# Kernel optimization log

Measured on AMD Instinct MI355X. Metric: run time of the kernel, lower is better.

The kernel has to match this reference:

```python
import jax, jax.numpy as jnp
import numpy as np

D_MODEL, D_K, D_V, HEADS = 512, 8, 8, 6
EPS = 1e-5


def setup_inputs() -> dict:
    key = jax.random.key(0)
    ks = jax.random.split(key, 16)
    B, S = 16, 1024
    inp = {
        'q_input': jax.random.normal(ks[0], (B, S, D_MODEL), jnp.float32),
        'k_input': jax.random.normal(ks[1], (B, S, D_MODEL), jnp.float32),
        'v_input': jax.random.normal(ks[2], (B, S, D_MODEL), jnp.float32),
        'mask': jax.random.randint(ks[3], (B, S, S), 0, 2).astype(bool),
        'Wq': jax.random.normal(ks[4], (D_MODEL, D_K * HEADS), jnp.float32) * 0.04,
        'bq': jax.random.normal(ks[5], (D_K * HEADS,), jnp.float32) * 0.02,
        'Wk': jax.random.normal(ks[6], (D_MODEL, D_K * HEADS), jnp.float32) * 0.04,
        'bk': jax.random.normal(ks[7], (D_K * HEADS,), jnp.float32) * 0.02,
        'Wv': jax.random.normal(ks[8], (D_MODEL, D_V * HEADS), jnp.float32) * 0.04,
        'bv': jax.random.normal(ks[9], (D_V * HEADS,), jnp.float32) * 0.02,
        'Wo': jax.random.normal(ks[10], (HEADS * D_K, D_MODEL), jnp.float32) * 0.1,
        'bo': jax.random.normal(ks[11], (D_MODEL,), jnp.float32) * 0.02,
        'ln_w': 1.0 + jax.random.normal(ks[12], (D_MODEL,), jnp.float32) * 0.02,
        'ln_b': jax.random.normal(ks[13], (D_MODEL,), jnp.float32) * 0.02,
    }
    return inp


def reference(q_input, k_input, v_input, mask, Wq, bq, Wk, bk, Wv, bv, Wo, bo, ln_w, ln_b):
    B, S, _ = q_input.shape
    # projections -> [B, H, S, d]
    q_s = (q_input @ Wq + bq).reshape(B, S, HEADS, D_K).transpose(0, 2, 1, 3)
    k_s = (k_input @ Wk + bk).reshape(B, S, HEADS, D_K).transpose(0, 2, 1, 3)
    v_s = (v_input @ Wv + bv).reshape(B, S, HEADS, D_V).transpose(0, 2, 1, 3)
    # scaled dot-product with masked_fill(mask, 1e-9) as in the original (fills VALUE, not -inf)
    scores = jnp.einsum('bhqd,bhkd->bhqk', q_s, k_s) / np.sqrt(D_K).astype(np.float32)
    scores = jnp.where(mask[:, None, :, :], jnp.float32(1e-9), scores)
    attn = jax.nn.softmax(scores, axis=-1)
    out = jnp.einsum('bhqk,bhkd->bhqd', attn, v_s)  # [B,H,S,d_v]
    out = out.transpose(0, 2, 1, 3).reshape(B, S, HEADS * D_K)
    out = out @ Wo + bo
    x = q_input + out  # residual
    mu = jnp.mean(x, axis=-1, keepdims=True)
    var = jnp.var(x, axis=-1, keepdims=True)
    return (x - mu) * jax.lax.rsqrt(var + EPS) * ln_w + ln_b
```

## Files before the change

### kernel.cpp

```cpp
#include <hip/hip_runtime.h>

constexpr int B = 16;
constexpr int S = 1024;
constexpr int DM = 512;
constexpr int H = 6;
constexpr int DK = 8;
constexpr int NJ = H * DK;
constexpr int BS = B * S;
constexpr int WB_ELEMS = 16 * NJ * 32;

typedef __attribute__((ext_vector_type(8))) short bf16x8;
typedef __attribute__((ext_vector_type(8))) _Float16 half8;
typedef __attribute__((ext_vector_type(4))) float floatx4;

#define LOG2E 1.4426950408889634f
#define QSCALE (0.35355339059327373f * LOG2E)

__device__ inline ushort f2bf(float f) {
  unsigned int u = __builtin_bit_cast(unsigned int, f);
  return (ushort)((u + 0x7FFFu + ((u >> 16) & 1u)) >> 16);
}

__global__ __launch_bounds__(256) void maskbits_kernel(
    const int* __restrict__ mask, unsigned long long* __restrict__ bits) {
  int wave = threadIdx.x >> 6, lane = threadIdx.x & 63;
  int row = blockIdx.x * 4 + wave;
  const int* mrow = mask + (size_t)row * S;
  unsigned long long* brow = bits + (size_t)row * 16;
#pragma unroll
  for (int c = 0; c < 16; c++) {
    int v = mrow[c * 64 + lane];
    unsigned long long bal = __ballot(v != 0);
    if (lane == 0) brow[c] = bal;
  }
}

__global__ __launch_bounds__(256) void wprep_kernel(
    const float* __restrict__ Wq, const float* __restrict__ Wk,
    const float* __restrict__ Wv, ushort* __restrict__ Wb) {
  int m = blockIdx.x;
  const float* W = (m == 0) ? Wq : (m == 1) ? Wk : Wv;
  ushort* dst = Wb + (size_t)m * WB_ELEMS;
  for (int e = threadIdx.x; e < WB_ELEMS; e += 256) {
    int kc = e / 1536;
    int rem = e - kc * 1536;
    int n = rem >> 5, kj = rem & 31;
    dst[e] = f2bf(W[(size_t)(kc * 32 + kj) * NJ + n]);
  }
}

__global__ __launch_bounds__(256) void proj_kernel(
    const float* __restrict__ q_in, const float* __restrict__ k_in,
    const float* __restrict__ v_in, const ushort* __restrict__ Wb,
    const float* __restrict__ bq, const float* __restrict__ bk,
    const float* __restrict__ bv,
    ushort* __restrict__ Qo, ushort* __restrict__ Ko, ushort* __restrict__ Vo) {
  int m = blockIdx.y;
  const float* x    = (m == 0) ? q_in : (m == 1) ? k_in : v_in;
  const float* bias = (m == 0) ? bq   : (m == 1) ? bk   : bv;
  ushort* out       = (m == 0) ? Qo   : (m == 1) ? Ko   : Vo;
  float oscale      = (m == 0) ? QSCALE : 1.0f;
  const ushort* Wg  = Wb + (size_t)m * WB_ELEMS;

  __shared__ ushort Wl[WB_ELEMS];

  int t = threadIdx.x;
  {
    const uint4* src = (const uint4*)Wg;
    uint4* dst = (uint4*)Wl;
#pragma unroll
    for (int i = 0; i < 12; i++) dst[t + i * 256] = src[t + i * 256];
  }

  int r0 = blockIdx.x * 64;
  int wave = t >> 6, lane = t & 63;
  int n16 = lane & 15, quad = lane >> 4;
  const float* xrow = x + (size_t)(r0 + wave * 16 + n16) * DM + quad * 8;

  floatx4 acc0 = {0.f, 0.f, 0.f, 0.f};
  floatx4 acc1 = {0.f, 0.f, 0.f, 0.f};
  floatx4 acc2 = {0.f, 0.f, 0.f, 0.f};

  __syncthreads();

#pragma unroll 4
  for (int kc = 0; kc < 16; kc++) {
    float4 xa = *(const float4*)(xrow + kc * 32);
    float4 xb = *(const float4*)(xrow + kc * 32 + 4);
    bf16x8 a;
    a[0] = (short)f2bf(xa.x); a[1] = (short)f2bf(xa.y);
    a[2] = (short)f2bf(xa.z); a[3] = (short)f2bf(xa.w);
    a[4] = (short)f2bf(xb.x); a[5] = (short)f2bf(xb.y);
    a[6] = (short)f2bf(xb.z); a[7] = (short)f2bf(xb.w);
    const ushort* wbase = &Wl[(kc * 48 + n16) * 32 + quad * 8];
    bf16x8 b0 = *(const bf16x8*)(wbase);
    bf16x8 b1 = *(const bf16x8*)(wbase + 16 * 32);
    bf16x8 b2 = *(const bf16x8*)(wbase + 32 * 32);
    acc0 = __builtin_amdgcn_mfma_f32_16x16x32_bf16(a, b0, acc0, 0, 0, 0);
    acc1 = __builtin_amdgcn_mfma_f32_16x16x32_bf16(a, b1, acc1, 0, 0, 0);
    acc2 = __builtin_amdgcn_mfma_f32_16x16x32_bf16(a, b2, acc2, 0, 0, 0);
  }

  int baseR = r0 + wave * 16 + quad * 4;
#pragma unroll
  for (int j = 0; j < 3; j++) {
    floatx4 a = (j == 0) ? acc0 : (j == 1) ? acc1 : acc2;
    int n = j * 16 + n16;
    float bn = bias[n];
    int h = n >> 3, d = n & 7;
#pragma unroll
    for (int r = 0; r < 4; r++) {
      int R = baseR + r;
      int b = R >> 10, s = R & 1023;
      float fv = (a[r] + bn) * oscale;
      ushort val = (m == 2) ? __builtin_bit_cast(ushort, (_Float16)fv)
                            : f2bf(fv);
      out[(((size_t)(b * H + h)) * S + s) * 8 + d] = val;
    }
  }
}

__global__ __launch_bounds__(256) void attn_kernel(
    const ushort* __restrict__ Qg, const ushort* __restrict__ Kg,
    const ushort* __restrict__ Vg ,
    const uint* __restrict__ bits32, float* __restrict__ A) {
  int bh = blockIdx.x >> 4;
  int qt = blockIdx.x & 15;
  int b = bh / H, h = bh % H;
  int q0 = qt * 64;

  __shared__ ushort Vt[9 * 1032];
  __shared__ uint Pb[4][16 * 20];

  int t = threadIdx.x;
  int wave = t >> 6, lane = t & 63;
  int quad = lane >> 4, n16 = lane & 15;

  const ushort* Kbase = Kg + (size_t)bh * S * 8;
  const ushort* Vbase = Vg + (size_t)bh * S * 8;

  bf16x8 aq = {0, 0, 0, 0, 0, 0, 0, 0};
  if (quad == 0)
    aq = *(const bf16x8*)&Qg[((size_t)bh * S + q0 + wave * 16 + n16) * 8];

#pragma unroll
  for (int i = 0; i < 8; i++) {
    int e = t + i * 256;
    int key = e >> 1, db = (e & 1) << 2;
    ushort4 v = *(const ushort4*)&Vbase[key * 8 + db];
    int g = (key & ~31) + 2 * (key & 15) + ((key >> 4) & 1);
    Vt[(db + 0) * 1032 + g] = v.x;
    Vt[(db + 1) * 1032 + g] = v.y;
    Vt[(db + 2) * 1032 + g] = v.z;
    Vt[(db + 3) * 1032 + g] = v.w;
  }
#pragma unroll
  for (int i = 0; i < 4; i++) Vt[8 * 1032 + t + i * 256] = 0x3C00;
  __syncthreads();

  floatx4 acc = {0.f, 0.f, 0.f, 0.f};
  const floatx4 zero = {0.f, 0.f, 0.f, 0.f};
  int row0 = wave * 16 + quad * 4;
  uint* prow = &Pb[wave][0];
  const uint* mbase = bits32 + ((size_t)(b * S + q0 + row0)) * 32;

#pragma unroll 1
  for (int cc = 0; cc < 8; cc++) {
    uint4 mr[4];
#pragma unroll
    for (int r = 0; r < 4; r++)
      mr[r] = *(const uint4*)(mbase + r * 32 + cc * 4);

#pragma unroll
    for (int ci = 0; ci < 4; ci++) {
      int c = cc * 4 + ci;
      bf16x8 bk0 = *(const bf16x8*)&Kbase[(size_t)(c * 32 + n16) * 8];
      bf16x8 bk1 = *(const bf16x8*)&Kbase[(size_t)(c * 32 + 16 + n16) * 8];
      floatx4 sc0 = __builtin_amdgcn_mfma_f32_16x16x32_bf16(aq, bk0, zero, 0, 0, 0);
      floatx4 sc1 = __builtin_amdgcn_mfma_f32_16x16x32_bf16(aq, bk1, zero, 0, 0, 0);

#pragma unroll
      for (int r = 0; r < 4; r++) {
        uint mw = (ci == 0) ? mr[r].x : (ci == 1) ? mr[r].y
                : (ci == 2) ? mr[r].z : mr[r].w;
        uint tt = mw >> n16;
        uint mexp = (tt & 0x10001u) * 0xFFFFu;
        float p0 = exp2f(fminf(sc0[r], 15.f));
        float p1 = exp2f(fminf(sc1[r], 15.f));
        uint pw = __builtin_bit_cast(uint, __builtin_amdgcn_cvt_pkrtz(p0, p1));
        pw = (mexp & 0x3C003C00u) | (~mexp & pw);
        prow[(quad * 4 + r) * 20 + n16] = pw;
      }

      half8 ap = *(const half8*)((const ushort*)prow + n16 * 40 + quad * 8);
      int dd = (n16 < 9) ? n16 : 8;
      half8 bv = *(const half8*)&Vt[dd * 1032 + c * 32 + quad * 8];
      acc = __builtin_amdgcn_mfma_f32_16x16x32_f16(ap, bv, acc, 0, 0, 0);
    }
  }

#pragma unroll
  for (int r = 0; r < 4; r++) {
    float dnm = __shfl(acc[r], (lane & 48) | 8, 64);
    if (n16 < 8) {
      int qg = q0 + wave * 16 + quad * 4 + r;
      A[((size_t)(b * S + qg)) * NJ + h * 8 + n16] = acc[r] / dnm;
    }
  }
}

__global__ __launch_bounds__(256) void out_ln_kernel(
    const float* __restrict__ A, const float* __restrict__ Wo,
    const float* __restrict__ bo, const float* __restrict__ qin,
    const float* __restrict__ lnw, const float* __restrict__ lnb,
    float* __restrict__ out) {
  int r0 = blockIdx.x * 8;
  int t = threadIdx.x;
  __shared__ float As[8 * NJ];
#pragma unroll
  for (int i = t; i < 8 * NJ; i += 256) As[i] = A[(size_t)r0 * NJ + i];
  __syncthreads();

  int c0 = t, c1 = t + 256;
  float acc0[8], acc1[8];
#pragma unroll
  for (int r = 0; r < 8; r++) { acc0[r] = 0.f; acc1[r] = 0.f; }

#pragma unroll 4
  for (int j = 0; j < NJ; j++) {
    float w0 = Wo[(size_t)j * DM + c0];
    float w1 = Wo[(size_t)j * DM + c1];
#pragma unroll
    for (int r = 0; r < 8; r++) {
      float a = As[r * NJ + j];
      acc0[r] += a * w0;
      acc1[r] += a * w1;
    }
  }

  float b0 = bo[c0], b1 = bo[c1];
  float y0[8], y1[8], ssum[8], sq[8];
#pragma unroll
  for (int r = 0; r < 8; r++) {
    y0[r] = acc0[r] + b0 + qin[(size_t)(r0 + r) * DM + c0];
    y1[r] = acc1[r] + b1 + qin[(size_t)(r0 + r) * DM + c1];
    ssum[r] = y0[r] + y1[r];
    sq[r] = y0[r] * y0[r] + y1[r] * y1[r];
  }

  int wave = t >> 6, lane = t & 63;
  __shared__ float reds[4][8], redq[4][8];
#pragma unroll
  for (int r = 0; r < 8; r++) {
    float s = ssum[r], qq = sq[r];
#pragma unroll
    for (int off = 32; off > 0; off >>= 1) {
      s += __shfl_xor(s, off, 64);
      qq += __shfl_xor(qq, off, 64);
    }
    if (lane == 0) { reds[wave][r] = s; redq[wave][r] = qq; }
  }
  __syncthreads();

  float lw0 = lnw[c0], lw1 = lnw[c1], lb0 = lnb[c0], lb1 = lnb[c1];
#pragma unroll
  for (int r = 0; r < 8; r++) {
    float s = (reds[0][r] + reds[1][r]) + (reds[2][r] + reds[3][r]);
    float qq = (redq[0][r] + redq[1][r]) + (redq[2][r] + redq[3][r]);
    float mu = s * (1.f / 512.f);
    float var = qq * (1.f / 512.f) - mu * mu;
    float rstd = rsqrtf(var + 1e-5f);
    out[(size_t)(r0 + r) * DM + c0] = (y0[r] - mu) * rstd * lw0 + lb0;
    out[(size_t)(r0 + r) * DM + c1] = (y1[r] - mu) * rstd * lw1 + lb1;
  }
}

extern "C" void kernel_launch(void* const* d_in, const int* in_sizes, int n_in,
                              void* d_out, int out_size, void* d_ws,
                              size_t ws_size, hipStream_t stream) {
  const float* q_in = (const float*)d_in[0];
  const float* k_in = (const float*)d_in[1];
  const float* v_in = (const float*)d_in[2];
  const int* mask = (const int*)d_in[3];
  const float* Wq = (const float*)d_in[4];
  const float* bq = (const float*)d_in[5];
  const float* Wk = (const float*)d_in[6];
  const float* bk = (const float*)d_in[7];
  const float* Wv = (const float*)d_in[8];
  const float* bv = (const float*)d_in[9];
  const float* Wo = (const float*)d_in[10];
  const float* bo = (const float*)d_in[11];
  const float* lnw = (const float*)d_in[12];
  const float* lnb = (const float*)d_in[13];
  float* out = (float*)d_out;

  constexpr size_t QKV = (size_t)B * H * S * DK;
  ushort* base = (ushort*)d_ws;
  ushort* Qw = base;
  ushort* Kw = base + QKV;
  ushort* Vw = base + 2 * QKV;
  float* Aw = (float*)(base + 3 * QKV);
  unsigned long long* bits = (unsigned long long*)(Aw + (size_t)BS * NJ);
  ushort* Wb = (ushort*)(bits + (size_t)BS * 16);

  maskbits_kernel<<<BS / 4, 256, 0, stream>>>(mask, bits);
  wprep_kernel<<<3, 256, 0, stream>>>(Wq, Wk, Wv, Wb);
  proj_kernel<<<dim3(BS / 64, 3), 256, 0, stream>>>(
      q_in, k_in, v_in, Wb, bq, bk, bv, Qw, Kw, Vw);
  attn_kernel<<<(B * H * S) / 64, 256, 0, stream>>>(
      Qw, Kw, Vw, (const uint*)bits, Aw);
  out_ln_kernel<<<BS / 8, 256, 0, stream>>>(Aw, Wo, bo, q_in, lnw, lnb, out);
}
```

Baseline: 304.4 us.

## Keep attention probabilities in registers by computing transposed scores and pre-laid-out V

The attention kernel now computes K·Q^T so each lane's score outputs line up directly as the A-operand of a 16x16x16 f16 MFMA. This removes the per-iteration LDS round trip for probabilities and the shared-memory V transpose. The V projection writes fp16 straight into an MFMA-fragment layout with a ones column for the denominator, filled by wprep. Mask bits are permuted at pack time to match the new key ordering. The launch bound is set to 6 blocks per CU. The cost is doubled V workspace, strided V stores, and more global V traffic per block.

```diff
diff --git a/kernel.cpp b/kernel.cpp
--- a/kernel.cpp
+++ b/kernel.cpp
@@ -11,6 +11,7 @@
 
 typedef __attribute__((ext_vector_type(8))) short bf16x8;
 typedef __attribute__((ext_vector_type(8))) _Float16 half8;
+typedef __attribute__((ext_vector_type(4))) _Float16 half4;
 typedef __attribute__((ext_vector_type(4))) float floatx4;
 
 #define LOG2E 1.4426950408889634f
@@ -27,9 +28,10 @@
   int row = blockIdx.x * 4 + wave;
   const int* mrow = mask + (size_t)row * S;
   unsigned long long* brow = bits + (size_t)row * 16;
+  int koff = ((lane >> 5) << 5) + 2 * (lane & 15) + ((lane >> 4) & 1);
 #pragma unroll
   for (int c = 0; c < 16; c++) {
-    int v = mrow[c * 64 + lane];
+    int v = mrow[c * 64 + koff];
     unsigned long long bal = __ballot(v != 0);
     if (lane == 0) brow[c] = bal;
   }
@@ -37,15 +39,28 @@
 
 __global__ __launch_bounds__(256) void wprep_kernel(
     const float* __restrict__ Wq, const float* __restrict__ Wk,
-    const float* __restrict__ Wv, ushort* __restrict__ Wb) {
+    const float* __restrict__ Wv, ushort* __restrict__ Wb,
+    uint2* __restrict__ VBf) {
   int m = blockIdx.x;
-  const float* W = (m == 0) ? Wq : (m == 1) ? Wk : Wv;
-  ushort* dst = Wb + (size_t)m * WB_ELEMS;
-  for (int e = threadIdx.x; e < WB_ELEMS; e += 256) {
-    int kc = e / 1536;
-    int rem = e - kc * 1536;
-    int n = rem >> 5, kj = rem & 31;
-    dst[e] = f2bf(W[(size_t)(kc * 32 + kj) * NJ + n]);
+  if (m < 3) {
+    const float* W = (m == 0) ? Wq : (m == 1) ? Wk : Wv;
+    ushort* dst = Wb + (size_t)m * WB_ELEMS;
+    for (int e = threadIdx.x; e < WB_ELEMS; e += 256) {
+      int kc = e / 1536;
+      int rem = e - kc * 1536;
+      int n = rem >> 5, kj = rem & 31;
+      dst[e] = f2bf(W[(size_t)(kc * 32 + kj) * NJ + n]);
+    }
+  } else {
+    int bh = m - 3;
+    for (int i = threadIdx.x; i < 2048; i += 256) {
+      int tile = i >> 5;
+      int li = i & 31;
+      int g = li >> 3, dd = 8 + (li & 7);
+      uint hv = (dd == 8) ? 0x3C003C00u : 0u;
+      uint2 val; val.x = hv; val.y = hv;
+      VBf[((size_t)bh * 64 + tile) * 64 + g * 16 + dd] = val;
+    }
   }
 }
 
@@ -113,98 +128,98 @@
       int R = baseR + r;
       int b = R >> 10, s = R & 1023;
       float fv = (a[r] + bn) * oscale;
-      ushort val = (m == 2) ? __builtin_bit_cast(ushort, (_Float16)fv)
-                            : f2bf(fv);
-      out[(((size_t)(b * H + h)) * S + s) * 8 + d] = val;
-    }
-  }
-}
-
-__global__ __launch_bounds__(256) void attn_kernel(
+      if (m == 2) {
+        size_t idx =
+            ((((size_t)(b * H + h) * 64 + (s >> 4)) * 64) +
+             ((s >> 2) & 3) * 16 + d) * 4 + (s & 3);
+        out[idx] = __builtin_bit_cast(ushort, (_Float16)fv);
+      } else {
+        out[(((size_t)(b * H + h)) * S + s) * 8 + d] = f2bf(fv);
+      }
+    }
+  }
+}
+
+__global__ __launch_bounds__(256, 6) void attn_kernel(
     const ushort* __restrict__ Qg, const ushort* __restrict__ Kg,
-    const ushort* __restrict__ Vg ,
+    const ushort* __restrict__ VBg ,
     const uint* __restrict__ bits32, float* __restrict__ A) {
   int bh = blockIdx.x >> 4;
   int qt = blockIdx.x & 15;
   int b = bh / H, h = bh % H;
   int q0 = qt * 64;
 
-  __shared__ ushort Vt[9 * 1032];
-  __shared__ uint Pb[4][16 * 20];
-
   int t = threadIdx.x;
   int wave = t >> 6, lane = t & 63;
   int quad = lane >> 4, n16 = lane & 15;
 
   const ushort* Kbase = Kg + (size_t)bh * S * 8;
-  const ushort* Vbase = Vg + (size_t)bh * S * 8;
+  const uint2* VB = (const uint2*)VBg + (size_t)bh * (64 * 64);
 
   bf16x8 aq = {0, 0, 0, 0, 0, 0, 0, 0};
   if (quad == 0)
     aq = *(const bf16x8*)&Qg[((size_t)bh * S + q0 + wave * 16 + n16) * 8];
 
-#pragma unroll
-  for (int i = 0; i < 8; i++) {
-    int e = t + i * 256;
-    int key = e >> 1, db = (e & 1) << 2;
-    ushort4 v = *(const ushort4*)&Vbase[key * 8 + db];
-    int g = (key & ~31) + 2 * (key & 15) + ((key >> 4) & 1);
-    Vt[(db + 0) * 1032 + g] = v.x;
-    Vt[(db + 1) * 1032 + g] = v.y;
-    Vt[(db + 2) * 1032 + g] = v.z;
-    Vt[(db + 3) * 1032 + g] = v.w;
-  }
-#pragma unroll
-  for (int i = 0; i < 4; i++) Vt[8 * 1032 + t + i * 256] = 0x3C00;
-  __syncthreads();
-
-  floatx4 acc = {0.f, 0.f, 0.f, 0.f};
+  const uint* mrow = bits32 + (size_t)(b * S + q0 + wave * 16 + n16) * 32;
+
+  floatx4 acc0 = {0.f, 0.f, 0.f, 0.f};
+  floatx4 acc1 = {0.f, 0.f, 0.f, 0.f};
   const floatx4 zero = {0.f, 0.f, 0.f, 0.f};
-  int row0 = wave * 16 + quad * 4;
-  uint* prow = &Pb[wave][0];
-  const uint* mbase = bits32 + ((size_t)(b * S + q0 + row0)) * 32;
+  int sh0 = 2 * quad;
 
 #pragma unroll 1
   for (int cc = 0; cc < 8; cc++) {
-    uint4 mr[4];
-#pragma unroll
-    for (int r = 0; r < 4; r++)
-      mr[r] = *(const uint4*)(mbase + r * 32 + cc * 4);
-
+    uint4 mq = *(const uint4*)(mrow + cc * 4);
 #pragma unroll
     for (int ci = 0; ci < 4; ci++) {
       int c = cc * 4 + ci;
-      bf16x8 bk0 = *(const bf16x8*)&Kbase[(size_t)(c * 32 + n16) * 8];
-      bf16x8 bk1 = *(const bf16x8*)&Kbase[(size_t)(c * 32 + 16 + n16) * 8];
-      floatx4 sc0 = __builtin_amdgcn_mfma_f32_16x16x32_bf16(aq, bk0, zero, 0, 0, 0);
-      floatx4 sc1 = __builtin_amdgcn_mfma_f32_16x16x32_bf16(aq, bk1, zero, 0, 0, 0);
-
-#pragma unroll
-      for (int r = 0; r < 4; r++) {
-        uint mw = (ci == 0) ? mr[r].x : (ci == 1) ? mr[r].y
-                : (ci == 2) ? mr[r].z : mr[r].w;
-        uint tt = mw >> n16;
-        uint mexp = (tt & 0x10001u) * 0xFFFFu;
-        float p0 = exp2f(fminf(sc0[r], 15.f));
-        float p1 = exp2f(fminf(sc1[r], 15.f));
-        uint pw = __builtin_bit_cast(uint, __builtin_amdgcn_cvt_pkrtz(p0, p1));
-        pw = (mexp & 0x3C003C00u) | (~mexp & pw);
-        prow[(quad * 4 + r) * 20 + n16] = pw;
-      }
-
-      half8 ap = *(const half8*)((const ushort*)prow + n16 * 40 + quad * 8);
-      int dd = (n16 < 9) ? n16 : 8;
-      half8 bv = *(const half8*)&Vt[dd * 1032 + c * 32 + quad * 8];
-      acc = __builtin_amdgcn_mfma_f32_16x16x32_f16(ap, bv, acc, 0, 0, 0);
+      uint mw = (ci == 0) ? mq.x : (ci == 1) ? mq.y : (ci == 2) ? mq.z : mq.w;
+
+      bf16x8 ak0 = *(const bf16x8*)&Kbase[(size_t)(c * 32 + n16) * 8];
+      bf16x8 ak1 = *(const bf16x8*)&Kbase[(size_t)(c * 32 + 16 + n16) * 8];
+      uint2 vb0 = VB[(2 * c) * 64 + lane];
+      uint2 vb1 = VB[(2 * c + 1) * 64 + lane];
+
+      floatx4 s0 = __builtin_amdgcn_mfma_f32_16x16x32_bf16(ak0, aq, zero, 0, 0, 0);
+      floatx4 s1 = __builtin_amdgcn_mfma_f32_16x16x32_bf16(ak1, aq, zero, 0, 0, 0);
+
+      float p0 = exp2f(fminf(s0[0], 15.f)), p1 = exp2f(fminf(s0[1], 15.f));
+      float p2 = exp2f(fminf(s0[2], 15.f)), p3 = exp2f(fminf(s0[3], 15.f));
+      float p4 = exp2f(fminf(s1[0], 15.f)), p5 = exp2f(fminf(s1[1], 15.f));
+      float p6 = exp2f(fminf(s1[2], 15.f)), p7 = exp2f(fminf(s1[3], 15.f));
+      uint w0 = __builtin_bit_cast(uint, __builtin_amdgcn_cvt_pkrtz(p0, p1));
+      uint w1 = __builtin_bit_cast(uint, __builtin_amdgcn_cvt_pkrtz(p2, p3));
+      uint w2 = __builtin_bit_cast(uint, __builtin_amdgcn_cvt_pkrtz(p4, p5));
+      uint w3 = __builtin_bit_cast(uint, __builtin_amdgcn_cvt_pkrtz(p6, p7));
+
+      uint m0 = ((mw >> sh0) & 0x10001u) * 0xFFFFu;
+      uint m1 = ((mw >> (sh0 + 1)) & 0x10001u) * 0xFFFFu;
+      uint m2 = ((mw >> (sh0 + 8)) & 0x10001u) * 0xFFFFu;
+      uint m3 = ((mw >> (sh0 + 9)) & 0x10001u) * 0xFFFFu;
+      w0 = (m0 & 0x3C003C00u) | (~m0 & w0);
+      w1 = (m1 & 0x3C003C00u) | (~m1 & w1);
+      w2 = (m2 & 0x3C003C00u) | (~m2 & w2);
+      w3 = (m3 & 0x3C003C00u) | (~m3 & w3);
+
+      uint2 pu0; pu0.x = w0; pu0.y = w1;
+      uint2 pu1; pu1.x = w2; pu1.y = w3;
+      half4 pa0 = __builtin_bit_cast(half4, pu0);
+      half4 pa1 = __builtin_bit_cast(half4, pu1);
+
+      acc0 = __builtin_amdgcn_mfma_f32_16x16x16f16(
+          pa0, __builtin_bit_cast(half4, vb0), acc0, 0, 0, 0);
+      acc1 = __builtin_amdgcn_mfma_f32_16x16x16f16(
+          pa1, __builtin_bit_cast(half4, vb1), acc1, 0, 0, 0);
     }
   }
 
 #pragma unroll
   for (int r = 0; r < 4; r++) {
-    float dnm = __shfl(acc[r], (lane & 48) | 8, 64);
+    float sum = acc0[r] + acc1[r];
+    float dnm = __shfl(sum, (lane & 48) | 8, 64);
     if (n16 < 8) {
       int qg = q0 + wave * 16 + quad * 4 + r;
-      A[((size_t)(b * S + qg)) * NJ + h * 8 + n16] = acc[r] / dnm;
+      A[((size_t)(b * S + qg)) * NJ + h * 8 + n16] = sum / dnm;
     }
   }
 }
@@ -298,16 +313,16 @@
   ushort* base = (ushort*)d_ws;
   ushort* Qw = base;
   ushort* Kw = base + QKV;
-  ushort* Vw = base + 2 * QKV;
-  float* Aw = (float*)(base + 3 * QKV);
+  ushort* VBw = base + 2 * QKV;
+  float* Aw = (float*)(base + 4 * QKV);
   unsigned long long* bits = (unsigned long long*)(Aw + (size_t)BS * NJ);
   ushort* Wb = (ushort*)(bits + (size_t)BS * 16);
 
   maskbits_kernel<<<BS / 4, 256, 0, stream>>>(mask, bits);
-  wprep_kernel<<<3, 256, 0, stream>>>(Wq, Wk, Wv, Wb);
+  wprep_kernel<<<3 + B * H, 256, 0, stream>>>(Wq, Wk, Wv, Wb, (uint2*)VBw);
   proj_kernel<<<dim3(BS / 64, 3), 256, 0, stream>>>(
-      q_in, k_in, v_in, Wb, bq, bk, bv, Qw, Kw, Vw);
+      q_in, k_in, v_in, Wb, bq, bk, bv, Qw, Kw, VBw);
   attn_kernel<<<(B * H * S) / 64, 256, 0, stream>>>(
-      Qw, Kw, Vw, (const uint*)bits, Aw);
+      Qw, Kw, VBw, (const uint*)bits, Aw);
   out_ln_kernel<<<BS / 8, 256, 0, stream>>>(Aw, Wo, bo, q_in, lnw, lnb, out);
 }
```

New measurement: 305.9 us. Within noise of the previous version (+0.5%).
